# Optimization experiments

Measured on AMD Instinct MI355X. Metric: run time of the kernel, lower is better.

The kernel has to match this reference:

```python
import jax, jax.numpy as jnp
import numpy as np

R_ACT = 8
GROUPS = 32
EPS = 1e-5


def _group_norm(x, gamma, beta):
    # x: [B, C, T]; GroupNorm over (C//G, T) per group, per sample
    B, C, T = x.shape
    xr = x.reshape(B, GROUPS, C // GROUPS, T)
    mu = xr.mean(axis=(2, 3), keepdims=True)
    var = xr.var(axis=(2, 3), keepdims=True)
    xn = ((xr - mu) * jax.lax.rsqrt(var + EPS)).reshape(B, C, T)
    return xn * gamma[None, :, None] + beta[None, :, None]


def _topk_mean(logits, valid_len):
    # logits: [B, T, C]; valid_len: [B] int32. mean of top-k per class, k = max(1, valid_len // r_act)
    B, T, C = logits.shape
    vals = -jnp.sort(-logits, axis=1)            # descending sort along T
    csum = jnp.cumsum(vals, axis=1)              # [B, T, C]
    k = jnp.maximum(1, valid_len // R_ACT).astype(jnp.int32)  # [B]
    idx = jnp.broadcast_to((k - 1)[:, None, None], (B, 1, C))
    sel = jnp.take_along_axis(csum, idx, axis=1)[:, 0, :]     # [B, C]
    return sel / k[:, None].astype(logits.dtype)


def setup_inputs() -> dict:
    key = jax.random.key(0)
    ks = jax.random.split(key, 12)
    B, Fd, T, O, Timg, D, C = 16, 2048, 2048, 512, 2048, 512, 20
    inp = {
        "input_features": jax.random.normal(ks[0], (B, Fd, T), jnp.float32),
        "masks": jnp.ones((B, 1, T), jnp.float32),
        "text_proto": jax.random.normal(ks[1], (1, C, D), jnp.float32),
        "img_feats": jax.random.normal(ks[2], (B, Timg, D), jnp.float32),
        "img_masks": jnp.ones((B, Timg), jnp.float32),
        # 1x1-conv embedding params (2 layers) + GN affines + cls linear
        "W1": jax.random.normal(ks[3], (O, Fd), jnp.float32) * 0.02,
        "b1": jnp.zeros((O,), jnp.float32),
        "g1": jnp.ones((O,), jnp.float32),
        "beta1": jnp.zeros((O,), jnp.float32),
        "W2": jax.random.normal(ks[4], (O, O), jnp.float32) * 0.02,
        "b2": jnp.zeros((O,), jnp.float32),
        "g2": jnp.ones((O,), jnp.float32),
        "beta2": jnp.zeros((O,), jnp.float32),
        "Wc": jax.random.normal(ks[5], (C, O), jnp.float32) * 0.02,
        "bc": jnp.zeros((C,), jnp.float32),
    }
    return inp


def reference(input_features, masks, text_proto, img_feats, img_masks,
              W1, b1, g1, beta1, W2, b2, g2, beta2, Wc, bc):
    # feature embedding: two (1x1 conv -> GN) blocks, mask applied after each
    x = jnp.einsum('of,bft->bot', W1, input_features) + b1[None, :, None]
    x = _group_norm(x, g1, beta1) * masks
    x = jnp.einsum('oc,bct->bot', W2, x) + b2[None, :, None]
    x = _group_norm(x, g2, beta2) * masks            # [B, O, T]
    fe = x.transpose(0, 2, 1)                        # [B, T, O]
    cls_logits = jax.nn.sigmoid(jnp.einsum('bto,co->btc', fe, Wc) + bc)  # [B, T, C]

    tp = text_proto[0].T                             # [D, C]
    text_logits = jnp.einsum('btd,dc->btc', img_feats, tp)  # [B, Timg, C]

    text_len = jax.lax.stop_gradient(img_masks).sum(-1).astype(jnp.int32)      # [B]
    cls_len = jax.lax.stop_gradient(masks).sum(axis=(-2, -1)).astype(jnp.int32)  # [B]
    text_vid_scores = _topk_mean(text_logits, text_len)  # [B, C]
    cls_vid_scores = _topk_mean(cls_logits, cls_len)     # [B, C]
    # stack both heads: [0] = text (inference output), [1] = cls (training output)
    return jnp.stack([text_vid_scores, cls_vid_scores])
```

## Files before the change

### kernel.cpp

```cpp
#include <hip/hip_runtime.h>

typedef unsigned short u16;
typedef unsigned int u32;
typedef unsigned long long u64;

typedef __attribute__((ext_vector_type(8))) __bf16 bf16x8;
typedef __attribute__((ext_vector_type(4))) float f32x4;

__device__ __forceinline__ u16 f2bf(float f) {
  u32 u = __float_as_uint(f);
  u = (u + 0x7fffu + ((u >> 16) & 1u)) >> 16;
  return (u16)u;
}
__device__ __forceinline__ float bf2f(u16 h) {
  return __uint_as_float(((u32)h) << 16);
}

__device__ __forceinline__ void stage16(const u16* g, u16* lds_wave_base) {
#if __has_builtin(__builtin_amdgcn_global_load_lds)
  __builtin_amdgcn_global_load_lds((__attribute__((address_space(1))) u32*)g,
                                   (__attribute__((address_space(3))) u32*)lds_wave_base,
                                   16, 0, 0);
#else
  u16* l = lds_wave_base + (threadIdx.x & 63) * 8;
  *(uint4*)l = *(const uint4*)g;
#endif
}

__device__ __forceinline__ float wred(float v) {
  v += __shfl_xor(v, 1, 64);
  v += __shfl_xor(v, 2, 64);
  v += __shfl_xor(v, 4, 64);
  v += __shfl_xor(v, 8, 64);
  v += __shfl_xor(v, 16, 64);
  v += __shfl_xor(v, 32, 64);
  return v;
}

__global__ void __launch_bounds__(256) f2bf_kernel(const float* __restrict__ in,
                                                   u16* __restrict__ out, int n4) {
  int i = blockIdx.x * 256 + threadIdx.x;
  if (i >= n4) return;
  float4 v = ((const float4*)in)[i];
  u64 p = (u64)f2bf(v.x) | ((u64)f2bf(v.y) << 16) | ((u64)f2bf(v.z) << 32) |
          ((u64)f2bf(v.w) << 48);
  ((u64*)out)[i] = p;
}

__global__ void __launch_bounds__(256) transpose_bf16(const float* __restrict__ src,
                                                      u16* __restrict__ dst,
                                                      long long fStride, long long oStride) {
  __shared__ float tile[64][65];
  int b = blockIdx.z;
  const float* s = src + (size_t)b * fStride;
  u16* d = dst + (size_t)b * oStride;
  int tid = threadIdx.x;
  int t0 = blockIdx.x * 64, f0 = blockIdx.y * 64;
  int r = tid >> 2, cq = (tid & 3) * 16;
#pragma unroll
  for (int q = 0; q < 4; ++q) {
    float4 v = *(const float4*)(s + (size_t)(f0 + r) * 2048 + (t0 + cq + q * 4));
    tile[r][cq + q * 4 + 0] = v.x;
    tile[r][cq + q * 4 + 1] = v.y;
    tile[r][cq + q * 4 + 2] = v.z;
    tile[r][cq + q * 4 + 3] = v.w;
  }
  __syncthreads();
  u32 ow[8];
#pragma unroll
  for (int h = 0; h < 8; ++h) {
    float lo = tile[cq + 2 * h + 0][r];
    float hi = tile[cq + 2 * h + 1][r];
    ow[h] = (u32)f2bf(lo) | ((u32)f2bf(hi) << 16);
  }
  u16* dp = d + (size_t)(t0 + r) * 2048 + f0 + cq;
  uint4 v0 = {ow[0], ow[1], ow[2], ow[3]};
  uint4 v1 = {ow[4], ow[5], ow[6], ow[7]};
  *(uint4*)dp = v0;
  *(uint4*)(dp + 8) = v1;
}

#define BAR() __builtin_amdgcn_s_barrier()
#define LGKM0() asm volatile("s_waitcnt lgkmcnt(0)" ::: "memory")
#define VMC4() asm volatile("s_waitcnt vmcnt(4)" ::: "memory")
#define VMC0() asm volatile("s_waitcnt vmcnt(0)" ::: "memory")

__device__ __forceinline__ void rdA4(const u16 (&sAb)[256][32], int mh, int wm, int ln, int sl,
                                     bf16x8 (&af)[4]) {
#pragma unroll
  for (int mi = 0; mi < 4; ++mi)
    af[mi] = *(const bf16x8*)&sAb[wm * 128 + mh * 64 + mi * 16 + ln][sl];
}
__device__ __forceinline__ void rdB4(const u16 (&sBb)[256][32], int wn, int ln, int sl,
                                     bf16x8 (&bfr)[4]) {
#pragma unroll
  for (int ni = 0; ni < 4; ++ni)
    bfr[ni] = *(const bf16x8*)&sBb[wn * 64 + ni * 16 + ln][sl];
}
__device__ __forceinline__ void mfma8(f32x4 (&acc)[8][4], const bf16x8 (&af)[4],
                                      const bf16x8 (&bfr)[4], int mh) {
  __builtin_amdgcn_s_setprio(1);
#pragma unroll
  for (int mi = 0; mi < 4; ++mi)
#pragma unroll
    for (int ni = 0; ni < 4; ++ni)
      acc[mh * 4 + mi][ni] = __builtin_amdgcn_mfma_f32_16x16x32_bf16(
          af[mi], bfr[ni], acc[mh * 4 + mi][ni], 0, 0, 0);
  __builtin_amdgcn_s_setprio(0);
}
__device__ __forceinline__ void stg2(const u16* g0, const u16* g1, u16 (&dst)[256][32],
                                     int wid, int koff) {
  stage16(g0 + koff, &dst[wid * 32][0]);
  stage16(g1 + koff, &dst[wid * 32 + 16][0]);
}

__global__ void __launch_bounds__(512, 2) gemm8(const u16* __restrict__ A,
                                                const u16* __restrict__ A0,
                                                const u16* __restrict__ Bw,
                                                const float* __restrict__ bias,
                                                u16* __restrict__ Out,
                                                int M, int N, int K) {
  __shared__ u16 sA[2][2][256][32];
  __shared__ u16 sB[2][2][256][32];
  int tid = threadIdx.x;
  int bz = blockIdx.z;
  int m0 = blockIdx.x * 256, n0 = blockIdx.y * 256;
  const u16* Ab = (bz == 0) ? A0 : (A + (size_t)bz * M * K);
  int lane = tid & 63, wid = tid >> 6;
  int wm = wid >> 2, wn = wid & 3;
  int ln = lane & 15, lm = lane >> 4;
  int sl = (lm ^ (ln & 3)) * 8;
  int lrow = lane >> 2;
  int swz = (lane & 3) ^ (lrow & 3);
  const u16* gA0 = Ab + (size_t)(m0 + wid * 32 + lrow) * K + swz * 8;
  const u16* gA1 = gA0 + (size_t)16 * K;
  const u16* gB0 = Bw + (size_t)(n0 + wid * 32 + lrow) * K + swz * 8;
  const u16* gB1 = gB0 + (size_t)16 * K;

  f32x4 acc[8][4];
#pragma unroll
  for (int mi = 0; mi < 8; ++mi)
#pragma unroll
    for (int ni = 0; ni < 4; ++ni) acc[mi][ni] = (f32x4){0.f, 0.f, 0.f, 0.f};

  bf16x8 af[4], bfr[4];

  stg2(gA0, gA1, sA[0][0], wid, 0);
  stg2(gB0, gB1, sB[0][0], wid, 0);
  stg2(gA0, gA1, sA[0][1], wid, 32);
  stg2(gB0, gB1, sB[0][1], wid, 32);
  stg2(gA0, gA1, sA[1][0], wid, 64);
  stg2(gB0, gB1, sB[1][0], wid, 64);
  VMC4();
  BAR();

  int NI = K >> 7;
  int kt0 = 0;
  for (int I = 0; I < NI - 1; ++I, kt0 += 2) {
    int kb1 = (kt0 + 1) * 64 + 32;
    int kb2 = (kt0 + 2) * 64;
    int kb3 = (kt0 + 2) * 64 + 32;
    int kb4 = (kt0 + 3) * 64;
    rdB4(sB[0][0], wn, ln, sl, bfr);
    rdA4(sA[0][0], 0, wm, ln, sl, af);
    stg2(gA0, gA1, sA[1][1], wid, kb1);
    BAR(); LGKM0(); mfma8(acc, af, bfr, 0); BAR();
    rdA4(sA[0][0], 1, wm, ln, sl, af);
    stg2(gB0, gB1, sB[1][1], wid, kb1);
    BAR(); LGKM0(); mfma8(acc, af, bfr, 1); BAR();
    rdB4(sB[0][1], wn, ln, sl, bfr);
    rdA4(sA[0][1], 0, wm, ln, sl, af);
    stg2(gA0, gA1, sA[0][0], wid, kb2);
    BAR(); LGKM0(); mfma8(acc, af, bfr, 0); BAR();
    rdA4(sA[0][1], 1, wm, ln, sl, af);
    stg2(gB0, gB1, sB[0][0], wid, kb2);
    BAR(); LGKM0(); mfma8(acc, af, bfr, 1);
    VMC4(); BAR();
    rdB4(sB[1][0], wn, ln, sl, bfr);
    rdA4(sA[1][0], 0, wm, ln, sl, af);
    stg2(gA0, gA1, sA[0][1], wid, kb3);
    BAR(); LGKM0(); mfma8(acc, af, bfr, 0); BAR();
    rdA4(sA[1][0], 1, wm, ln, sl, af);
    stg2(gB0, gB1, sB[0][1], wid, kb3);
    BAR(); LGKM0(); mfma8(acc, af, bfr, 1); BAR();
    rdB4(sB[1][1], wn, ln, sl, bfr);
    rdA4(sA[1][1], 0, wm, ln, sl, af);
    stg2(gA0, gA1, sA[1][0], wid, kb4);
    BAR(); LGKM0(); mfma8(acc, af, bfr, 0); BAR();
    rdA4(sA[1][1], 1, wm, ln, sl, af);
    stg2(gB0, gB1, sB[1][0], wid, kb4);
    BAR(); LGKM0(); mfma8(acc, af, bfr, 1);
    VMC4(); BAR();
  }
  {
    int kb1 = (kt0 + 1) * 64 + 32;
    rdB4(sB[0][0], wn, ln, sl, bfr);
    rdA4(sA[0][0], 0, wm, ln, sl, af);
    stg2(gA0, gA1, sA[1][1], wid, kb1);
    BAR(); LGKM0(); mfma8(acc, af, bfr, 0); BAR();
    rdA4(sA[0][0], 1, wm, ln, sl, af);
    stg2(gB0, gB1, sB[1][1], wid, kb1);
    BAR(); LGKM0(); mfma8(acc, af, bfr, 1); BAR();
    rdB4(sB[0][1], wn, ln, sl, bfr);
    rdA4(sA[0][1], 0, wm, ln, sl, af);
    BAR(); LGKM0(); mfma8(acc, af, bfr, 0); BAR();
    rdA4(sA[0][1], 1, wm, ln, sl, af);
    BAR(); LGKM0(); mfma8(acc, af, bfr, 1);
    VMC0(); BAR();
    rdB4(sB[1][0], wn, ln, sl, bfr);
    rdA4(sA[1][0], 0, wm, ln, sl, af);
    BAR(); LGKM0(); mfma8(acc, af, bfr, 0); BAR();
    rdA4(sA[1][0], 1, wm, ln, sl, af);
    BAR(); LGKM0(); mfma8(acc, af, bfr, 1); BAR();
    rdB4(sB[1][1], wn, ln, sl, bfr);
    rdA4(sA[1][1], 0, wm, ln, sl, af);
    BAR(); LGKM0(); mfma8(acc, af, bfr, 0); BAR();
    rdA4(sA[1][1], 1, wm, ln, sl, af);
    LGKM0(); mfma8(acc, af, bfr, 1);
  }

  float biasv[4];
#pragma unroll
  for (int ni = 0; ni < 4; ++ni) biasv[ni] = bias[n0 + wn * 64 + ni * 16 + ln];
  u16* ob = Out + (size_t)bz * M * N;
#pragma unroll
  for (int mi = 0; mi < 8; ++mi) {
    int mrow = m0 + wm * 128 + mi * 16 + lm * 4;
#pragma unroll
    for (int ni = 0; ni < 4; ++ni) {
      int ncol = n0 + wn * 64 + ni * 16 + ln;
#pragma unroll
      for (int r = 0; r < 4; ++r)
        ob[(size_t)(mrow + r) * N + ncol] = f2bf(acc[mi][ni][r] + biasv[ni]);
    }
  }
}

template <bool APPLY>
__global__ void __launch_bounds__(1024) gn_kernel(u16* __restrict__ x,
                                                  const float* __restrict__ gamma,
                                                  const float* __restrict__ beta,
                                                  const float* __restrict__ masks,
                                                  float* __restrict__ gmaOut,
                                                  float* __restrict__ gadOut) {
  const int T = 2048;
  int b = blockIdx.x >> 4, gp = blockIdx.x & 15;
  int tid = threadIdx.x;
  int sub = tid & 3, row = tid >> 2;
  int g = sub >> 1;
  u16* base = x + ((size_t)b * T * 512 + gp * 32);
  float s = 0.f, ss = 0.f;
#pragma unroll
  for (int it = 0; it < 8; ++it) {
    int t = it * 256 + row;
    uint4 v = *(const uint4*)(base + (size_t)t * 512 + sub * 8);
    u32 wv[4] = {v.x, v.y, v.z, v.w};
#pragma unroll
    for (int h = 0; h < 4; ++h) {
      float lo = bf2f((u16)(wv[h] & 0xffffu));
      float hi = bf2f((u16)(wv[h] >> 16));
      s += lo + hi;
      ss += lo * lo + hi * hi;
    }
  }
  s += __shfl_xor(s, 1, 64);  ss += __shfl_xor(ss, 1, 64);
  s += __shfl_xor(s, 4, 64);  ss += __shfl_xor(ss, 4, 64);
  s += __shfl_xor(s, 8, 64);  ss += __shfl_xor(ss, 8, 64);
  s += __shfl_xor(s, 16, 64); ss += __shfl_xor(ss, 16, 64);
  s += __shfl_xor(s, 32, 64); ss += __shfl_xor(ss, 32, 64);
  __shared__ float rs[16][2], rss[16][2], mu_s[2], inv_s[2];
  int wv_ = tid >> 6, lane = tid & 63;
  if (lane == 0 || lane == 2) { rs[wv_][g] = s; rss[wv_][g] = ss; }
  __syncthreads();
  if (tid < 2) {
    float S = 0.f, SS = 0.f;
#pragma unroll
    for (int wq = 0; wq < 16; ++wq) { S += rs[wq][tid]; SS += rss[wq][tid]; }
    float cnt = 16.f * (float)T;
    float mu = S / cnt;
    float var = SS / cnt - mu * mu;
    mu_s[tid] = mu;
    inv_s[tid] = rsqrtf(var + 1e-5f);
  }
  __syncthreads();
  if constexpr (APPLY) {
    float mu = mu_s[g], inv = inv_s[g];
    float gm[8], bt[8];
#pragma unroll
    for (int j = 0; j < 8; ++j) {
      int ch = gp * 32 + sub * 8 + j;
      gm[j] = gamma[ch] * inv;
      bt[j] = beta[ch] - mu * gm[j];
    }
#pragma unroll
    for (int it = 0; it < 8; ++it) {
      int t = it * 256 + row;
      u16* p = base + (size_t)t * 512 + sub * 8;
      uint4 v = *(const uint4*)p;
      float mk = masks[(size_t)b * T + t];
      u32 wv2[4] = {v.x, v.y, v.z, v.w};
      u32 ow[4];
#pragma unroll
      for (int h = 0; h < 4; ++h) {
        float lo = bf2f((u16)(wv2[h] & 0xffffu));
        float hi = bf2f((u16)(wv2[h] >> 16));
        lo = (lo * gm[2 * h] + bt[2 * h]) * mk;
        hi = (hi * gm[2 * h + 1] + bt[2 * h + 1]) * mk;
        ow[h] = (u32)f2bf(lo) | ((u32)f2bf(hi) << 16);
      }
      uint4 o4 = {ow[0], ow[1], ow[2], ow[3]};
      *(uint4*)p = o4;
    }
  } else {
    if (tid < 32) {
      int ch = gp * 32 + tid;
      int gg = tid >> 4;
      float gm = gamma[ch] * inv_s[gg];
      gmaOut[(size_t)b * 512 + ch] = gm;
      gadOut[(size_t)b * 512 + ch] = beta[ch] - mu_s[gg] * gm;
    }
  }
}

template <typename TX, bool CLS>
__global__ void __launch_bounds__(512) head_v2(const TX* __restrict__ X,
                                               const float* __restrict__ W,
                                               const float* __restrict__ bcv,
                                               const float* __restrict__ gma,
                                               const float* __restrict__ gad,
                                               const float* __restrict__ masks,
                                               float* __restrict__ Out, int Tdim) {
  __shared__ float red[64 * 20];
  int tid = threadIdx.x;
  int tl = tid & 63;
  int ks = __builtin_amdgcn_readfirstlane(tid >> 6);
  int b = blockIdx.y;
  int t = blockIdx.x * 64 + tl;
  for (int i = tid; i < 64 * 20; i += 512) red[i] = 0.f;
  float acc[20];
#pragma unroll
  for (int c = 0; c < 20; ++c) acc[c] = 0.f;
  const TX* xr = X + ((size_t)b * Tdim + t) * 512 + ks * 64;
  const float* Wk = W + ks * 64;
  const float* gmk = CLS ? (gma + (size_t)b * 512 + ks * 64) : nullptr;
  const float* gak = CLS ? (gad + (size_t)b * 512 + ks * 64) : nullptr;
  __syncthreads();
#pragma unroll
  for (int kk = 0; kk < 64; kk += 8) {
    float xv[8];
    if constexpr (sizeof(TX) == 2) {
      uint4 v = *(const uint4*)(xr + kk);
      u32 wv[4] = {v.x, v.y, v.z, v.w};
#pragma unroll
      for (int h = 0; h < 4; ++h) {
        xv[2 * h] = bf2f((u16)(wv[h] & 0xffffu));
        xv[2 * h + 1] = bf2f((u16)(wv[h] >> 16));
      }
    } else {
      float4 p0 = *(const float4*)(xr + kk);
      float4 p1 = *(const float4*)(xr + kk + 4);
      xv[0] = p0.x; xv[1] = p0.y; xv[2] = p0.z; xv[3] = p0.w;
      xv[4] = p1.x; xv[5] = p1.y; xv[6] = p1.z; xv[7] = p1.w;
    }
    if constexpr (CLS) {
#pragma unroll
      for (int j = 0; j < 8; ++j) xv[j] = xv[j] * gmk[kk + j] + gak[kk + j];
    }
#pragma unroll
    for (int c = 0; c < 20; ++c) {
      const float* wr = &Wk[c * 512 + kk];
#pragma unroll
      for (int j = 0; j < 8; ++j) acc[c] += xv[j] * wr[j];
    }
  }
#pragma unroll
  for (int c = 0; c < 20; ++c) atomicAdd(&red[tl * 20 + c], acc[c]);
  __syncthreads();
  if (tid < 64) {
    float mk = CLS ? masks[(size_t)b * Tdim + t] : 1.f;
#pragma unroll
    for (int c = 0; c < 20; ++c) {
      float v = red[tid * 20 + c];
      if constexpr (CLS) {
        v = v * mk + bcv[c];
        v = 1.f / (1.f + __expf(-v));
      }
      Out[((size_t)b * 20 + c) * Tdim + t] = v;
    }
  }
}

__global__ void __launch_bounds__(256) topk_kernel(const float* __restrict__ textL,
                                                   const float* __restrict__ clsL,
                                                   const float* __restrict__ img_masks,
                                                   const float* __restrict__ masks,
                                                   float* __restrict__ out) {
  __shared__ float d[2048];
  __shared__ float rbuf[4];
  int bx = blockIdx.x;
  int head = bx / 320, rem = bx - head * 320;
  int b = rem / 20, c = rem - b * 20;
  int tid = threadIdx.x;
  const float* mk = head ? (masks + (size_t)b * 2048) : (img_masks + (size_t)b * 2048);
  float ls = 0.f;
  for (int i = tid; i < 2048; i += 256) ls += mk[i];
  ls = wred(ls);
  if ((tid & 63) == 0) rbuf[tid >> 6] = ls;
  const float* rowp = (head ? clsL : textL) + ((size_t)(b * 20 + c)) * 2048;
  for (int i = tid; i < 2048; i += 256) d[i] = rowp[i];
  __syncthreads();
  int len = (int)(rbuf[0] + rbuf[1] + rbuf[2] + rbuf[3]);
  int k = len >> 3;
  if (k < 1) k = 1;
  for (int size = 2; size <= 2048; size <<= 1) {
    for (int stride = size >> 1; stride > 0; stride >>= 1) {
      __syncthreads();
      for (int i = tid; i < 2048; i += 256) {
        int j = i ^ stride;
        if (j > i) {
          float a = d[i], bb = d[j];
          bool desc = ((i & size) == 0);
          if (desc ? (a < bb) : (a > bb)) { d[i] = bb; d[j] = a; }
        }
      }
    }
  }
  __syncthreads();
  float ps = 0.f;
  for (int i = tid; i < k; i += 256) ps += d[i];
  ps = wred(ps);
  __syncthreads();
  if ((tid & 63) == 0) rbuf[tid >> 6] = ps;
  __syncthreads();
  if (tid == 0) out[bx] = (rbuf[0] + rbuf[1] + rbuf[2] + rbuf[3]) / (float)k;
}

extern "C" void kernel_launch(void* const* d_in, const int* in_sizes, int n_in,
                              void* d_out, int out_size, void* d_ws, size_t ws_size,
                              hipStream_t stream) {
  const float* F          = (const float*)d_in[0];
  const float* masks      = (const float*)d_in[1];
  const float* text_proto = (const float*)d_in[2];
  const float* img_feats  = (const float*)d_in[3];
  const float* img_masks  = (const float*)d_in[4];
  const float* W1 = (const float*)d_in[5];
  const float* b1 = (const float*)d_in[6];
  const float* g1 = (const float*)d_in[7];
  const float* be1 = (const float*)d_in[8];
  const float* W2 = (const float*)d_in[9];
  const float* b2 = (const float*)d_in[10];
  const float* g2 = (const float*)d_in[11];
  const float* be2 = (const float*)d_in[12];
  const float* Wc = (const float*)d_in[13];
  const float* bc = (const float*)d_in[14];
  float* out = (float*)d_out;

  const int T = 2048, Fd = 2048, O = 512;
  char* w = (char*)d_ws;
  u16* W1b     = (u16*)(w);
  u16* W2b     = (u16*)(w + 2097152);
  u16* x1      = (u16*)(w + 2621440);
  float* clsL  = (float*)(w + 36175872);
  float* textL = (float*)(w + 38797312);
  float* gma   = (float*)(w + 41418752);
  float* gad   = (float*)(w + 41451520);
  const size_t oEnd0 = 41484288;
  const size_t ftBytes = (size_t)16 * T * Fd * 2;

  f2bf_kernel<<<1024, 256, 0, stream>>>(W1, W1b, (O * Fd) / 4);
  f2bf_kernel<<<256, 256, 0, stream>>>(W2, W2b, (O * O) / 4);

  const u16 *FtA, *FtA0;
  u16* x2;
  if (ws_size >= oEnd0 + ftBytes) {
    u16* Ft = (u16*)(w + oEnd0);
    transpose_bf16<<<dim3(32, 32, 16), 256, 0, stream>>>(F, Ft, (long long)Fd * T,
                                                         (long long)T * Fd);
    FtA = Ft; FtA0 = Ft; x2 = Ft;
  } else {
    u16* ft0 = (u16*)(w + oEnd0);
    x2 = (u16*)(w + oEnd0 + (size_t)T * Fd * 2);
    for (int b = 0; b < 16; ++b) {
      u16* dst = (b == 0) ? ft0 : ((u16*)d_in[0]) + (size_t)b * T * Fd;
      transpose_bf16<<<dim3(32, 32, 1), 256, 0, stream>>>(F + (size_t)b * Fd * T, dst, 0, 0);
    }
    FtA = (const u16*)d_in[0]; FtA0 = ft0;
  }

  gemm8<<<dim3(8, 2, 16), 512, 0, stream>>>(FtA, FtA0, W1b, b1, x1, 2048, 512, 2048);
  gn_kernel<true><<<256, 1024, 0, stream>>>(x1, g1, be1, masks, nullptr, nullptr);
  gemm8<<<dim3(8, 2, 16), 512, 0, stream>>>(x1, x1, W2b, b2, x2, 2048, 512, 512);
  gn_kernel<false><<<256, 1024, 0, stream>>>(x2, g2, be2, masks, gma, gad);
  head_v2<u16, true><<<dim3(32, 16), 512, 0, stream>>>(x2, Wc, bc, gma, gad, masks, clsL, 2048);
  head_v2<float, false><<<dim3(32, 16), 512, 0, stream>>>(img_feats, text_proto, nullptr,
                                                          nullptr, nullptr, nullptr, textL, 2048);
  topk_kernel<<<640, 256, 0, stream>>>(textL, clsL, img_masks, masks, out);
}
```

Measured before the change: 757.0 us.

## Fuse GroupNorm stats into GEMM epilogues, fold GN1 into W2, radix-select top-k

```diff
diff --git a/kernel.cpp b/kernel.cpp
--- a/kernel.cpp
+++ b/kernel.cpp
@@ -45,6 +45,11 @@
   u64 p = (u64)f2bf(v.x) | ((u64)f2bf(v.y) << 16) | ((u64)f2bf(v.z) << 32) |
           ((u64)f2bf(v.w) << 48);
   ((u64*)out)[i] = p;
+}
+
+__global__ void __launch_bounds__(256) zinit(float* __restrict__ p, int n) {
+  int i = blockIdx.x * 256 + threadIdx.x;
+  if (i < n) p[i] = 0.f;
 }
 
 __global__ void __launch_bounds__(256) transpose_bf16(const float* __restrict__ src,
@@ -114,10 +119,16 @@
   stage16(g1 + koff, &dst[wid * 32 + 16][0]);
 }
 
+template <bool MASKED>
 __global__ void __launch_bounds__(512, 2) gemm8(const u16* __restrict__ A,
                                                 const u16* __restrict__ A0,
                                                 const u16* __restrict__ Bw,
-                                                const float* __restrict__ bias,
+                                                size_t bStride,
+                                                const float* __restrict__ t1,
+                                                const float* __restrict__ t2,
+                                                const float* __restrict__ mkp,
+                                                float* __restrict__ sOut,
+                                                float* __restrict__ ssOut,
                                                 u16* __restrict__ Out,
                                                 int M, int N, int K) {
   __shared__ u16 sA[2][2][256][32];
@@ -126,6 +137,7 @@
   int bz = blockIdx.z;
   int m0 = blockIdx.x * 256, n0 = blockIdx.y * 256;
   const u16* Ab = (bz == 0) ? A0 : (A + (size_t)bz * M * K);
+  const u16* Bb = Bw + (size_t)bz * bStride;
   int lane = tid & 63, wid = tid >> 6;
   int wm = wid >> 2, wn = wid & 3;
   int ln = lane & 15, lm = lane >> 4;
@@ -134,7 +146,7 @@
   int swz = (lane & 3) ^ (lrow & 3);
   const u16* gA0 = Ab + (size_t)(m0 + wid * 32 + lrow) * K + swz * 8;
   const u16* gA1 = gA0 + (size_t)16 * K;
-  const u16* gB0 = Bw + (size_t)(n0 + wid * 32 + lrow) * K + swz * 8;
+  const u16* gB0 = Bb + (size_t)(n0 + wid * 32 + lrow) * K + swz * 8;
   const u16* gB1 = gB0 + (size_t)16 * K;
 
   f32x4 acc[8][4];
@@ -219,107 +231,97 @@
     LGKM0(); mfma8(acc, af, bfr, 1);
   }
 
-  float biasv[4];
-#pragma unroll
-  for (int ni = 0; ni < 4; ++ni) biasv[ni] = bias[n0 + wn * 64 + ni * 16 + ln];
+  const float* t1p = MASKED ? (t1 + (size_t)bz * N) : t1;
+  float t1v[4], t2v[4];
+#pragma unroll
+  for (int ni = 0; ni < 4; ++ni) {
+    int ncol = n0 + wn * 64 + ni * 16 + ln;
+    t1v[ni] = t1p[ncol];
+    t2v[ni] = MASKED ? t2[ncol] : 0.f;
+  }
+  float sp[4] = {0.f, 0.f, 0.f, 0.f}, ssp[4] = {0.f, 0.f, 0.f, 0.f};
   u16* ob = Out + (size_t)bz * M * N;
 #pragma unroll
   for (int mi = 0; mi < 8; ++mi) {
     int mrow = m0 + wm * 128 + mi * 16 + lm * 4;
+    float mka[4] = {1.f, 1.f, 1.f, 1.f};
+    if constexpr (MASKED) {
+      float4 mv = *(const float4*)(mkp + (size_t)bz * M + mrow);
+      mka[0] = mv.x; mka[1] = mv.y; mka[2] = mv.z; mka[3] = mv.w;
+    }
 #pragma unroll
     for (int ni = 0; ni < 4; ++ni) {
       int ncol = n0 + wn * 64 + ni * 16 + ln;
 #pragma unroll
-      for (int r = 0; r < 4; ++r)
-        ob[(size_t)(mrow + r) * N + ncol] = f2bf(acc[mi][ni][r] + biasv[ni]);
-    }
-  }
-}
-
-template <bool APPLY>
-__global__ void __launch_bounds__(1024) gn_kernel(u16* __restrict__ x,
-                                                  const float* __restrict__ gamma,
-                                                  const float* __restrict__ beta,
-                                                  const float* __restrict__ masks,
-                                                  float* __restrict__ gmaOut,
-                                                  float* __restrict__ gadOut) {
-  const int T = 2048;
-  int b = blockIdx.x >> 4, gp = blockIdx.x & 15;
-  int tid = threadIdx.x;
-  int sub = tid & 3, row = tid >> 2;
-  int g = sub >> 1;
-  u16* base = x + ((size_t)b * T * 512 + gp * 32);
-  float s = 0.f, ss = 0.f;
-#pragma unroll
-  for (int it = 0; it < 8; ++it) {
-    int t = it * 256 + row;
-    uint4 v = *(const uint4*)(base + (size_t)t * 512 + sub * 8);
-    u32 wv[4] = {v.x, v.y, v.z, v.w};
-#pragma unroll
-    for (int h = 0; h < 4; ++h) {
-      float lo = bf2f((u16)(wv[h] & 0xffffu));
-      float hi = bf2f((u16)(wv[h] >> 16));
-      s += lo + hi;
-      ss += lo * lo + hi * hi;
-    }
-  }
-  s += __shfl_xor(s, 1, 64);  ss += __shfl_xor(ss, 1, 64);
-  s += __shfl_xor(s, 4, 64);  ss += __shfl_xor(ss, 4, 64);
-  s += __shfl_xor(s, 8, 64);  ss += __shfl_xor(ss, 8, 64);
-  s += __shfl_xor(s, 16, 64); ss += __shfl_xor(ss, 16, 64);
-  s += __shfl_xor(s, 32, 64); ss += __shfl_xor(ss, 32, 64);
-  __shared__ float rs[16][2], rss[16][2], mu_s[2], inv_s[2];
-  int wv_ = tid >> 6, lane = tid & 63;
-  if (lane == 0 || lane == 2) { rs[wv_][g] = s; rss[wv_][g] = ss; }
-  __syncthreads();
-  if (tid < 2) {
-    float S = 0.f, SS = 0.f;
-#pragma unroll
-    for (int wq = 0; wq < 16; ++wq) { S += rs[wq][tid]; SS += rss[wq][tid]; }
-    float cnt = 16.f * (float)T;
-    float mu = S / cnt;
-    float var = SS / cnt - mu * mu;
-    mu_s[tid] = mu;
-    inv_s[tid] = rsqrtf(var + 1e-5f);
-  }
-  __syncthreads();
-  if constexpr (APPLY) {
-    float mu = mu_s[g], inv = inv_s[g];
-    float gm[8], bt[8];
-#pragma unroll
-    for (int j = 0; j < 8; ++j) {
-      int ch = gp * 32 + sub * 8 + j;
-      gm[j] = gamma[ch] * inv;
-      bt[j] = beta[ch] - mu * gm[j];
-    }
-#pragma unroll
-    for (int it = 0; it < 8; ++it) {
-      int t = it * 256 + row;
-      u16* p = base + (size_t)t * 512 + sub * 8;
-      uint4 v = *(const uint4*)p;
-      float mk = masks[(size_t)b * T + t];
-      u32 wv2[4] = {v.x, v.y, v.z, v.w};
-      u32 ow[4];
-#pragma unroll
-      for (int h = 0; h < 4; ++h) {
-        float lo = bf2f((u16)(wv2[h] & 0xffffu));
-        float hi = bf2f((u16)(wv2[h] >> 16));
-        lo = (lo * gm[2 * h] + bt[2 * h]) * mk;
-        hi = (hi * gm[2 * h + 1] + bt[2 * h + 1]) * mk;
-        ow[h] = (u32)f2bf(lo) | ((u32)f2bf(hi) << 16);
+      for (int r = 0; r < 4; ++r) {
+        float v = acc[mi][ni][r] + t1v[ni];
+        if constexpr (MASKED) v = v * mka[r] + t2v[ni];
+        sp[ni] += v;
+        ssp[ni] += v * v;
+        ob[(size_t)(mrow + r) * N + ncol] = f2bf(v);
       }
-      uint4 o4 = {ow[0], ow[1], ow[2], ow[3]};
-      *(uint4*)p = o4;
-    }
-  } else {
-    if (tid < 32) {
-      int ch = gp * 32 + tid;
-      int gg = tid >> 4;
-      float gm = gamma[ch] * inv_s[gg];
-      gmaOut[(size_t)b * 512 + ch] = gm;
-      gadOut[(size_t)b * 512 + ch] = beta[ch] - mu_s[gg] * gm;
-    }
-  }
+    }
+  }
+#pragma unroll
+  for (int ni = 0; ni < 4; ++ni) {
+    float S = wred(sp[ni]);
+    float SS = wred(ssp[ni]);
+    if (lane == 0) {
+      int grp = blockIdx.y * 16 + wn * 4 + ni;
+      atomicAdd(&sOut[bz * 32 + grp], S);
+      atomicAdd(&ssOut[bz * 32 + grp], SS);
+    }
+  }
+}
+
+__global__ void __launch_bounds__(512) gnstats(const float* __restrict__ sS,
+                                               const float* __restrict__ sSS,
+                                               const float* __restrict__ gamma,
+                                               const float* __restrict__ beta,
+                                               float* __restrict__ gmO,
+                                               float* __restrict__ gdO) {
+  int b = blockIdx.x;
+  int c = threadIdx.x;
+  int g = c >> 4;
+  const float cnt = 16.f * 2048.f;
+  float mu = sS[b * 32 + g] / cnt;
+  float var = sSS[b * 32 + g] / cnt - mu * mu;
+  float inv = rsqrtf(var + 1e-5f);
+  float gm = gamma[c] * inv;
+  gmO[(size_t)b * 512 + c] = gm;
+  gdO[(size_t)b * 512 + c] = beta[c] - mu * gm;
+}
+
+__global__ void __launch_bounds__(256) wfold(const float* __restrict__ W2,
+                                             const float* __restrict__ gm1,
+                                             const float* __restrict__ bt1,
+                                             u16* __restrict__ W2f,
+                                             float* __restrict__ beta2) {
+  int w = blockIdx.x * 4 + (threadIdx.x >> 6);
+  int lane = threadIdx.x & 63;
+  int b = w >> 9, o = w & 511;
+  const float* wr = W2 + (size_t)o * 512 + lane * 8;
+  const float* gmr = gm1 + (size_t)b * 512 + lane * 8;
+  const float* btr = bt1 + (size_t)b * 512 + lane * 8;
+  float4 w0 = *(const float4*)wr, w1 = *(const float4*)(wr + 4);
+  float4 g0 = *(const float4*)gmr, g1v = *(const float4*)(gmr + 4);
+  float4 t0 = *(const float4*)btr, t1v = *(const float4*)(btr + 4);
+  float wv[8] = {w0.x, w0.y, w0.z, w0.w, w1.x, w1.y, w1.z, w1.w};
+  float gv[8] = {g0.x, g0.y, g0.z, g0.w, g1v.x, g1v.y, g1v.z, g1v.w};
+  float tv[8] = {t0.x, t0.y, t0.z, t0.w, t1v.x, t1v.y, t1v.z, t1v.w};
+  u32 ow[4];
+  float acc = 0.f;
+#pragma unroll
+  for (int h = 0; h < 4; ++h) {
+    float lo = wv[2 * h] * gv[2 * h];
+    float hi = wv[2 * h + 1] * gv[2 * h + 1];
+    ow[h] = (u32)f2bf(lo) | ((u32)f2bf(hi) << 16);
+    acc += wv[2 * h] * tv[2 * h] + wv[2 * h + 1] * tv[2 * h + 1];
+  }
+  uint4 o4 = {ow[0], ow[1], ow[2], ow[3]};
+  *(uint4*)(W2f + ((size_t)b * 512 + o) * 512 + lane * 8) = o4;
+  acc = wred(acc);
+  if (lane == 0) beta2[(size_t)b * 512 + o] = acc;
 }
 
 template <typename TX, bool CLS>
@@ -390,13 +392,15 @@
   }
 }
 
-__global__ void __launch_bounds__(256) topk_kernel(const float* __restrict__ textL,
-                                                   const float* __restrict__ clsL,
-                                                   const float* __restrict__ img_masks,
-                                                   const float* __restrict__ masks,
-                                                   float* __restrict__ out) {
-  __shared__ float d[2048];
-  __shared__ float rbuf[4];
+__global__ void __launch_bounds__(256) topk_sel(const float* __restrict__ textL,
+                                                const float* __restrict__ clsL,
+                                                const float* __restrict__ img_masks,
+                                                const float* __restrict__ masks,
+                                                float* __restrict__ out) {
+  __shared__ u32 keys[2048];
+  __shared__ u32 hist[256];
+  __shared__ u32 sel[2];
+  __shared__ float rbuf[4], rbuf2[4];
   int bx = blockIdx.x;
   int head = bx / 320, rem = bx - head * 320;
   int b = rem / 20, c = rem - b * 20;
@@ -407,32 +411,70 @@
   ls = wred(ls);
   if ((tid & 63) == 0) rbuf[tid >> 6] = ls;
   const float* rowp = (head ? clsL : textL) + ((size_t)(b * 20 + c)) * 2048;
-  for (int i = tid; i < 2048; i += 256) d[i] = rowp[i];
+  for (int i = tid; i < 2048; i += 256) {
+    u32 u = __float_as_uint(rowp[i]);
+    u32 sgn = (u32)((int)u >> 31);
+    keys[i] = u ^ (sgn | 0x80000000u);
+  }
   __syncthreads();
   int len = (int)(rbuf[0] + rbuf[1] + rbuf[2] + rbuf[3]);
-  int k = len >> 3;
+  u32 k = (u32)(len >> 3);
   if (k < 1) k = 1;
-  for (int size = 2; size <= 2048; size <<= 1) {
-    for (int stride = size >> 1; stride > 0; stride >>= 1) {
-      __syncthreads();
-      for (int i = tid; i < 2048; i += 256) {
-        int j = i ^ stride;
-        if (j > i) {
-          float a = d[i], bb = d[j];
-          bool desc = ((i & size) == 0);
-          if (desc ? (a < bb) : (a > bb)) { d[i] = bb; d[j] = a; }
-        }
+  u32 want = k, prefix = 0;
+#pragma unroll
+  for (int byt = 3; byt >= 0; --byt) {
+    int sh = byt * 8;
+    hist[tid] = 0;
+    __syncthreads();
+    for (int i = tid; i < 2048; i += 256) {
+      u32 kk = keys[i];
+      bool match = (byt == 3) || ((kk >> (sh + 8)) == (prefix >> (sh + 8)));
+      if (match) atomicAdd(&hist[(kk >> sh) & 0xffu], 1u);
+    }
+    __syncthreads();
+    if (tid < 64) {
+      int r0 = tid * 4;
+      u32 h0 = hist[255 - r0], h1 = hist[254 - r0], h2 = hist[253 - r0], h3 = hist[252 - r0];
+      u32 p0 = h0, p1 = p0 + h1, p2 = p1 + h2, p3 = p2 + h3;
+      u32 inc = p3;
+#pragma unroll
+      for (int off = 1; off < 64; off <<= 1) {
+        u32 t = __shfl_up(inc, off, 64);
+        if (tid >= off) inc += t;
       }
-    }
-  }
+      u32 excl = inc - p3;
+      u32 S0 = excl + p0, S1 = excl + p1, S2 = excl + p2, S3 = excl + p3;
+      if (S0 >= want && excl < want) { sel[0] = (u32)(255 - r0); sel[1] = want - excl; }
+      if (S1 >= want && S0 < want)   { sel[0] = (u32)(254 - r0); sel[1] = want - S0; }
+      if (S2 >= want && S1 < want)   { sel[0] = (u32)(253 - r0); sel[1] = want - S1; }
+      if (S3 >= want && S2 < want)   { sel[0] = (u32)(252 - r0); sel[1] = want - S2; }
+    }
+    __syncthreads();
+    prefix |= sel[0] << sh;
+    want = sel[1];
+    __syncthreads();
+  }
+  float s = 0.f, cg = 0.f;
+  for (int i = tid; i < 2048; i += 256) {
+    u32 kk = keys[i];
+    if (kk > prefix) {
+      u32 u = (kk & 0x80000000u) ? (kk ^ 0x80000000u) : ~kk;
+      s += __uint_as_float(u);
+      cg += 1.f;
+    }
+  }
+  s = wred(s);
+  cg = wred(cg);
+  if ((tid & 63) == 0) { rbuf[tid >> 6] = s; rbuf2[tid >> 6] = cg; }
   __syncthreads();
-  float ps = 0.f;
-  for (int i = tid; i < k; i += 256) ps += d[i];
-  ps = wred(ps);
-  __syncthreads();
-  if ((tid & 63) == 0) rbuf[tid >> 6] = ps;
-  __syncthreads();
-  if (tid == 0) out[bx] = (rbuf[0] + rbuf[1] + rbuf[2] + rbuf[3]) / (float)k;
+  if (tid == 0) {
+    float S = rbuf[0] + rbuf[1] + rbuf[2] + rbuf[3];
+    float CG = rbuf2[0] + rbuf2[1] + rbuf2[2] + rbuf2[3];
+    u32 u = (prefix & 0x80000000u) ? (prefix ^ 0x80000000u) : ~prefix;
+    float thr = __uint_as_float(u);
+    S += ((float)k - CG) * thr;
+    out[bx] = S / (float)k;
+  }
 }
 
 extern "C" void kernel_launch(void* const* d_in, const int* in_sizes, int n_in,
@@ -458,7 +500,6 @@
   const int T = 2048, Fd = 2048, O = 512;
   char* w = (char*)d_ws;
   u16* W1b     = (u16*)(w);
-  u16* W2b     = (u16*)(w + 2097152);
   u16* x1      = (u16*)(w + 2621440);
   float* clsL  = (float*)(w + 36175872);
   float* textL = (float*)(w + 38797312);
@@ -466,13 +507,24 @@
   float* gad   = (float*)(w + 41451520);
   const size_t oEnd0 = 41484288;
   const size_t ftBytes = (size_t)16 * T * Fd * 2;
+  const size_t EXTRA = 8388608 + 3 * 32768 + 8192;
+
+  bool bigws = ws_size >= oEnd0 + ftBytes + EXTRA;
+  char* ext = bigws ? (w + oEnd0 + ftBytes)
+                    : (w + oEnd0 + (size_t)T * Fd * 2 + (size_t)16 * T * O * 2);
+  u16* W2f    = (u16*)ext;
+  float* gm1  = (float*)(ext + 8388608);
+  float* bt1  = gm1 + 16 * 512;
+  float* beta2 = bt1 + 16 * 512;
+  float* sbase = beta2 + 16 * 512;
+  float* s1 = sbase, *ss1 = sbase + 512, *s2 = sbase + 1024, *ss2 = sbase + 1536;
 
   f2bf_kernel<<<1024, 256, 0, stream>>>(W1, W1b, (O * Fd) / 4);
-  f2bf_kernel<<<256, 256, 0, stream>>>(W2, W2b, (O * O) / 4);
+  zinit<<<8, 256, 0, stream>>>(sbase, 2048);
 
   const u16 *FtA, *FtA0;
   u16* x2;
-  if (ws_size >= oEnd0 + ftBytes) {
+  if (bigws) {
     u16* Ft = (u16*)(w + oEnd0);
     transpose_bf16<<<dim3(32, 32, 16), 256, 0, stream>>>(F, Ft, (long long)Fd * T,
                                                          (long long)T * Fd);
@@ -487,12 +539,15 @@
     FtA = (const u16*)d_in[0]; FtA0 = ft0;
   }
 
-  gemm8<<<dim3(8, 2, 16), 512, 0, stream>>>(FtA, FtA0, W1b, b1, x1, 2048, 512, 2048);
-  gn_kernel<true><<<256, 1024, 0, stream>>>(x1, g1, be1, masks, nullptr, nullptr);
-  gemm8<<<dim3(8, 2, 16), 512, 0, stream>>>(x1, x1, W2b, b2, x2, 2048, 512, 512);
-  gn_kernel<false><<<256, 1024, 0, stream>>>(x2, g2, be2, masks, gma, gad);
+  gemm8<false><<<dim3(8, 2, 16), 512, 0, stream>>>(FtA, FtA0, W1b, 0, b1, nullptr, nullptr,
+                                                   s1, ss1, x1, 2048, 512, 2048);
+  gnstats<<<16, 512, 0, stream>>>(s1, ss1, g1, be1, gm1, bt1);
+  wfold<<<2048, 256, 0, stream>>>(W2, gm1, bt1, W2f, beta2);
+  gemm8<true><<<dim3(8, 2, 16), 512, 0, stream>>>(x1, x1, W2f, (size_t)512 * 512, beta2, b2,
+                                                  masks, s2, ss2, x2, 2048, 512, 512);
+  gnstats<<<16, 512, 0, stream>>>(s2, ss2, g2, be2, gma, gad);
   head_v2<u16, true><<<dim3(32, 16), 512, 0, stream>>>(x2, Wc, bc, gma, gad, masks, clsL, 2048);
   head_v2<float, false><<<dim3(32, 16), 512, 0, stream>>>(img_feats, text_proto, nullptr,
                                                           nullptr, nullptr, nullptr, textL, 2048);
-  topk_kernel<<<640, 256, 0, stream>>>(textL, clsL, img_masks, masks, out);
-}
+  topk_sel<<<640, 256, 0, stream>>>(textL, clsL, img_masks, masks, out);
+}
```

Result: faster. 664.4 us (-12.2%).
